# Kernel optimization log

Hardware: AMD Instinct MI355X
Metric: run time of the kernel (lower is better)

Reference implementation:

```python
import jax, jax.numpy as jnp
import numpy as np

M, N, D, L = 32, 2048, 128, 32768
H = N // D


def setup_inputs() -> dict:
    key = jax.random.key(0)
    k1, k2, k3, k4 = jax.random.split(key, 4)
    X = jax.random.normal(k1, (M, N), dtype=jnp.float32)
    # 0.02 init keeps un-scaled (no 1/sqrt(D)) logits inside fp32 exp range
    W_qkv = jax.random.normal(k2, (N, 3 * N), dtype=jnp.float32) * 0.02
    cache_K = jax.random.normal(k3, (H, L, D), dtype=jnp.float32) * 0.1
    cache_V = jax.random.normal(k4, (H, L, D), dtype=jnp.float32) * 0.1
    return {"X": X, "W_qkv": W_qkv, "cache_K": cache_K, "cache_V": cache_V, "P": 16384}


def reference(X, W_qkv, cache_K, cache_V, P):
    m, n = X.shape
    h, l, d = cache_K.shape
    # RMSNorm without learned gain, eps=0 (faithful to source)
    variance = jnp.mean(X * X, axis=-1, keepdims=True)
    X_norm = X * jax.lax.rsqrt(variance)
    # fused QKV projection: [M, 3N]
    qkv = X_norm @ W_qkv
    q, k, v = jnp.split(qkv, 3, axis=-1)
    q = q.reshape(m, h, d).transpose(1, 0, 2)  # [H, M, D]
    k = k.reshape(m, h, d).transpose(1, 0, 2)
    v = v.reshape(m, h, d).transpose(1, 0, 2)
    # KV-cache write at position P (functional update)
    cache_K = jax.lax.dynamic_update_slice(cache_K, k, (0, P, 0))
    cache_V = jax.lax.dynamic_update_slice(cache_V, v, (0, P, 0))
    # naive (non-max-subtracted, unscaled) softmax attention over full cache
    scores = jnp.einsum("hmd,hld->hml", q, cache_K)  # [H, M, L]
    scores_exp = jnp.exp(scores)
    weights = scores_exp / jnp.sum(scores_exp, axis=-1, keepdims=True)
    out = jnp.einsum("hml,hld->hmd", weights, cache_V)  # [H, M, D]
    return out.transpose(1, 0, 2).reshape(m, h * d)
```

## Files before the change

### kernel.cpp

```cpp
#include <hip/hip_runtime.h>

#define MM 32
#define NN 2048
#define NJ 6144
#define HH 16
#define DD 128
#define LL 32768

typedef __attribute__((ext_vector_type(8))) short bf16x8;
typedef __attribute__((ext_vector_type(4))) short bf16x4s;
typedef __attribute__((ext_vector_type(4))) float f32x4;

static __device__ __forceinline__ short f2bf(float f) {
    union { float f; unsigned u; } v; v.f = f;
    unsigned r = v.u + 0x7FFFu + ((v.u >> 16) & 1u);
    return (short)(r >> 16);
}

__global__ __launch_bounds__(256) void k_rms(const float* __restrict__ X,
                                             float* __restrict__ xT) {
    const int m = blockIdx.x, t = threadIdx.x;
    const float4* xr = (const float4*)(X + m * NN);
    float4 a = xr[t * 2], b = xr[t * 2 + 1];
    float s = a.x*a.x + a.y*a.y + a.z*a.z + a.w*a.w
            + b.x*b.x + b.y*b.y + b.z*b.z + b.w*b.w;
    for (int o = 32; o; o >>= 1) s += __shfl_down(s, o);
    __shared__ float red[4];
    if ((t & 63) == 0) red[t >> 6] = s;
    __syncthreads();
    float rs = rsqrtf((red[0] + red[1] + red[2] + red[3]) * (1.0f / NN));
    int n0 = t * 8;
    xT[(n0 + 0) * MM + m] = a.x * rs;
    xT[(n0 + 1) * MM + m] = a.y * rs;
    xT[(n0 + 2) * MM + m] = a.z * rs;
    xT[(n0 + 3) * MM + m] = a.w * rs;
    xT[(n0 + 4) * MM + m] = b.x * rs;
    xT[(n0 + 5) * MM + m] = b.y * rs;
    xT[(n0 + 6) * MM + m] = b.z * rs;
    xT[(n0 + 7) * MM + m] = b.w * rs;
}

__global__ __launch_bounds__(256) void k_qkv(const float* __restrict__ xT,
                                             const float* __restrict__ W,
                                             float* __restrict__ part) {
    const int j = blockIdx.x * 256 + threadIdx.x;
    const int nc = blockIdx.y;
    const int n0 = nc * 128;
    float acc[32];
#pragma unroll
    for (int m = 0; m < 32; m++) acc[m] = 0.f;
#pragma unroll 4
    for (int i = 0; i < 128; i++) {
        const float* xr = xT + (size_t)(n0 + i) * MM;
        float w = W[(size_t)(n0 + i) * NJ + j];
#pragma unroll
        for (int m = 0; m < 32; m++) acc[m] += xr[m] * w;
    }
    float* o = part + (size_t)nc * (MM * NJ) + j;
#pragma unroll
    for (int m = 0; m < 32; m++) o[(size_t)m * NJ] = acc[m];
}

__global__ __launch_bounds__(256) void k_qkvred(const float* __restrict__ part,
                                                float* __restrict__ qkv) {
    const int idx = blockIdx.x * 256 + threadIdx.x;
    float s = 0.f;
#pragma unroll
    for (int c = 0; c < 16; c++) s += part[(size_t)c * (MM * NJ) + idx];
    qkv[idx] = s;
}

#define SMEM_D 54272
__global__ __launch_bounds__(256, 1) void k_attn(const float* __restrict__ cK,
                                                 const float* __restrict__ cV,
                                                 const float* __restrict__ qkv,
                                                 const int* __restrict__ Pp,
                                                 float* __restrict__ Opart,
                                                 float* __restrict__ Dpart) {
    extern __shared__ char smem[];
    const int h = blockIdx.x, sp = blockIdx.y;
    const int t = threadIdx.x, lane = t & 63, wave = t >> 6;
    short* q_s  = (short*)smem;
    short* kv_s = (short*)(smem + 8704) + wave * (32 * 136);
    short* w_s  = (short*)(smem + 43520) + wave * (32 * 40);
    float* dred = (float*)(smem + 53760);
    const int P = *Pp;

    {
        int m = t >> 3, db = (t & 7) * 16;
        const float4* src = (const float4*)(qkv + (size_t)m * NJ + h * DD + db);
        short* dst = q_s + m * 136 + db;
#pragma unroll
        for (int k = 0; k < 4; k++) {
            float4 v = src[k];
            bf16x4s o; o.x = f2bf(v.x); o.y = f2bf(v.y); o.z = f2bf(v.z); o.w = f2bf(v.w);
            *(bf16x4s*)(dst + 4 * k) = o;
        }
    }
    __syncthreads();

    const int l15 = lane & 15, q4 = lane >> 4;
    const int row_st = lane >> 5, col4 = (lane & 31) * 4;

    bf16x8 qf[2][4];
#pragma unroll
    for (int mt = 0; mt < 2; mt++)
#pragma unroll
        for (int kb = 0; kb < 4; kb++)
            qf[mt][kb] = *(const bf16x8*)(q_s + (mt * 16 + l15) * 136 + kb * 32 + q4 * 8);

    f32x4 acc[2][8];
#pragma unroll
    for (int mt = 0; mt < 2; mt++)
#pragma unroll
        for (int dt = 0; dt < 8; dt++) acc[mt][dt] = (f32x4){0.f, 0.f, 0.f, 0.f};
    float dacc[2][4] = {{0.f,0.f,0.f,0.f},{0.f,0.f,0.f,0.f}};

    for (int c = 0; c < 8; c++) {
        const int lbase = sp * 1024 + c * 128 + wave * 32;
        {
            const float* kb_ = cK + ((size_t)h * LL + lbase) * DD + col4;
#pragma unroll 4
            for (int p = 0; p < 16; p++) {
                int row = p * 2 + row_st;
                float4 v = *(const float4*)(kb_ + (size_t)row * DD);
                bf16x4s o; o.x = f2bf(v.x); o.y = f2bf(v.y); o.z = f2bf(v.z); o.w = f2bf(v.w);
                *(bf16x4s*)(kv_s + row * 136 + col4) = o;
            }
        }
#pragma unroll
        for (int lt = 0; lt < 2; lt++) {
            const int lcol = lbase + lt * 16 + l15;
            const bool masked = ((unsigned)(lcol - P)) < 32u;
#pragma unroll
            for (int mt = 0; mt < 2; mt++) {
                f32x4 s = (f32x4){0.f, 0.f, 0.f, 0.f};
#pragma unroll
                for (int kb2 = 0; kb2 < 4; kb2++) {
                    bf16x8 bfr = *(const bf16x8*)(kv_s + (lt * 16 + l15) * 136 + kb2 * 32 + q4 * 8);
                    s = __builtin_amdgcn_mfma_f32_16x16x32_bf16(qf[mt][kb2], bfr, s, 0, 0, 0);
                }
#pragma unroll
                for (int r = 0; r < 4; r++) {
                    float e = __expf(s[r]);
                    if (masked) e = 0.f;
                    dacc[mt][r] += e;
                    w_s[(mt * 16 + q4 * 4 + r) * 40 + lt * 16 + l15] = f2bf(e);
                }
            }
        }
        {
            const float* vb_ = cV + ((size_t)h * LL + lbase) * DD + col4;
#pragma unroll 4
            for (int p = 0; p < 16; p++) {
                int row = p * 2 + row_st;
                float4 v = *(const float4*)(vb_ + (size_t)row * DD);
                bf16x4s o; o.x = f2bf(v.x); o.y = f2bf(v.y); o.z = f2bf(v.z); o.w = f2bf(v.w);
                *(bf16x4s*)(kv_s + row * 136 + col4) = o;
            }
        }
        {
            bf16x8 a0 = *(const bf16x8*)(w_s + l15 * 40 + q4 * 8);
            bf16x8 a1 = *(const bf16x8*)(w_s + (16 + l15) * 40 + q4 * 8);
#pragma unroll
            for (int dt = 0; dt < 8; dt++) {
                bf16x8 bv;
#pragma unroll
                for (int jj = 0; jj < 8; jj++)
                    bv[jj] = kv_s[(q4 * 8 + jj) * 136 + dt * 16 + l15];
                acc[0][dt] = __builtin_amdgcn_mfma_f32_16x16x32_bf16(a0, bv, acc[0][dt], 0, 0, 0);
                acc[1][dt] = __builtin_amdgcn_mfma_f32_16x16x32_bf16(a1, bv, acc[1][dt], 0, 0, 0);
            }
        }
    }

#pragma unroll
    for (int mt = 0; mt < 2; mt++)
#pragma unroll
        for (int r = 0; r < 4; r++) {
            float v = dacc[mt][r];
            v += __shfl_xor(v, 1); v += __shfl_xor(v, 2);
            v += __shfl_xor(v, 4); v += __shfl_xor(v, 8);
            if (l15 == 0) dred[wave * 32 + mt * 16 + q4 * 4 + r] = v;
        }

    __syncthreads();
    float* buf = (float*)smem;
    if (wave < 2) {
        float* ob = buf + wave * 4096;
#pragma unroll
        for (int mt = 0; mt < 2; mt++)
#pragma unroll
            for (int dt = 0; dt < 8; dt++)
#pragma unroll
                for (int r = 0; r < 4; r++)
                    ob[(mt * 16 + q4 * 4 + r) * 128 + dt * 16 + l15] = acc[mt][dt][r];
    }
    __syncthreads();
    if (wave >= 2) {
        float* ob = buf + (wave - 2) * 4096;
#pragma unroll
        for (int mt = 0; mt < 2; mt++)
#pragma unroll
            for (int dt = 0; dt < 8; dt++)
#pragma unroll
                for (int r = 0; r < 4; r++)
                    ob[(mt * 16 + q4 * 4 + r) * 128 + dt * 16 + l15] += acc[mt][dt][r];
    }
    __syncthreads();
    float* Ob = Opart + ((size_t)h * 32 + sp) * 4096;
    for (int e = t; e < 4096; e += 256) Ob[e] = buf[e] + buf[4096 + e];
    if (t < 32) {
        float d = dred[t] + dred[32 + t] + dred[64 + t] + dred[96 + t];
        Dpart[((size_t)h * 32 + sp) * 32 + t] = d;
    }
}

__global__ __launch_bounds__(128) void k_final(const float* __restrict__ qkv,
                                               const float* __restrict__ Opart,
                                               const float* __restrict__ Dpart,
                                               float* __restrict__ out) {
    const int m = blockIdx.x, h = blockIdx.y, t = threadIdx.x;
    __shared__ float wnew[32];
    if (t < 32) {
        const float* qr = qkv + (size_t)m * NJ + h * DD;
        const float* kr = qkv + (size_t)t * NJ + 2048 + h * DD;
        float s = 0.f;
#pragma unroll 8
        for (int d = 0; d < 128; d++) s += qr[d] * kr[d];
        wnew[t] = __expf(s);
    }
    __syncthreads();
    const int d = t;
    float num = 0.f, den = 0.f;
#pragma unroll 4
    for (int m2 = 0; m2 < 32; m2++) {
        num += wnew[m2] * qkv[(size_t)m2 * NJ + 4096 + h * DD + d];
        den += wnew[m2];
    }
#pragma unroll 4
    for (int s2 = 0; s2 < 32; s2++) {
        num += Opart[(((size_t)h * 32 + s2) * 32 + m) * 128 + d];
        den += Dpart[((size_t)h * 32 + s2) * 32 + m];
    }
    out[(size_t)m * NN + h * DD + d] = num / den;
}

extern "C" void kernel_launch(void* const* d_in, const int* in_sizes, int n_in,
                              void* d_out, int out_size, void* d_ws, size_t ws_size,
                              hipStream_t stream) {
    const float* X  = (const float*)d_in[0];
    const float* W  = (const float*)d_in[1];
    const float* cK = (const float*)d_in[2];
    const float* cV = (const float*)d_in[3];
    const int*   Pp = (const int*)d_in[4];
    float* ws = (float*)d_ws;

    float* xT    = ws;
    float* qpart = ws + 65536;
    float* qkv   = ws + 3211264;
    float* Opart = ws + 3407872;
    float* Dpart = ws + 5505024;

    k_rms<<<32, 256, 0, stream>>>(X, xT);
    k_qkv<<<dim3(24, 16), 256, 0, stream>>>(xT, W, qpart);
    k_qkvred<<<768, 256, 0, stream>>>(qpart, qkv);
    k_attn<<<dim3(16, 32), 256, SMEM_D, stream>>>(cK, cV, qkv, Pp, Opart, Dpart);
    k_final<<<dim3(32, 16), 128, 0, stream>>>(qkv, Opart, Dpart, (float*)d_out);
}
```

Measured before the change: 585.9 us.

## Load K fragments directly into registers and prefetch next K chunk

K tiles are now loaded from global memory straight into MFMA fragment layout in registers, skipping the LDS staging round trip. The next chunk's K is prefetched while the current V tile is converted and the PV MFMAs run, and V loads are issued early into registers. Launch bounds are raised to allow two blocks per CU. This adds register pressure, which may cause spills under the tighter launch bound, and the K loads are now less coalesced (32-byte pieces per lane).

```diff
diff --git a/kernel.cpp b/kernel.cpp
--- a/kernel.cpp
+++ b/kernel.cpp
@@ -71,7 +71,7 @@
 }
 
 #define SMEM_D 54272
-__global__ __launch_bounds__(256, 1) void k_attn(const float* __restrict__ cK,
+__global__ __launch_bounds__(256, 2) void k_attn(const float* __restrict__ cK,
                                                  const float* __restrict__ cV,
                                                  const float* __restrict__ qkv,
                                                  const int* __restrict__ Pp,
@@ -81,10 +81,26 @@
     const int h = blockIdx.x, sp = blockIdx.y;
     const int t = threadIdx.x, lane = t & 63, wave = t >> 6;
     short* q_s  = (short*)smem;
-    short* kv_s = (short*)(smem + 8704) + wave * (32 * 136);
+    short* v_s  = (short*)(smem + 8704) + wave * (32 * 136);
     short* w_s  = (short*)(smem + 43520) + wave * (32 * 40);
     float* dred = (float*)(smem + 53760);
     const int P = *Pp;
+
+    const int l15 = lane & 15, q4 = lane >> 4;
+    const int row_st = lane >> 5, col4 = (lane & 31) * 4;
+
+    const float* kbase = cK + ((size_t)h * LL + sp * 1024 + wave * 32) * DD;
+    const float* vbase = cV + ((size_t)h * LL + sp * 1024 + wave * 32) * DD;
+
+    float4 kraw[2][4][2];
+#pragma unroll
+    for (int lt = 0; lt < 2; lt++)
+#pragma unroll
+        for (int kb = 0; kb < 4; kb++) {
+            const float* p0 = kbase + (size_t)(lt * 16 + l15) * DD + kb * 32 + q4 * 8;
+            kraw[lt][kb][0] = *(const float4*)p0;
+            kraw[lt][kb][1] = *(const float4*)(p0 + 4);
+        }
 
     {
         int m = t >> 3, db = (t & 7) * 16;
@@ -99,9 +115,6 @@
     }
     __syncthreads();
 
-    const int l15 = lane & 15, q4 = lane >> 4;
-    const int row_st = lane >> 5, col4 = (lane & 31) * 4;
-
     bf16x8 qf[2][4];
 #pragma unroll
     for (int mt = 0; mt < 2; mt++)
@@ -118,16 +131,27 @@
 
     for (int c = 0; c < 8; c++) {
         const int lbase = sp * 1024 + c * 128 + wave * 32;
+
+        float4 vraw[16];
         {
-            const float* kb_ = cK + ((size_t)h * LL + lbase) * DD + col4;
-#pragma unroll 4
-            for (int p = 0; p < 16; p++) {
-                int row = p * 2 + row_st;
-                float4 v = *(const float4*)(kb_ + (size_t)row * DD);
-                bf16x4s o; o.x = f2bf(v.x); o.y = f2bf(v.y); o.z = f2bf(v.z); o.w = f2bf(v.w);
-                *(bf16x4s*)(kv_s + row * 136 + col4) = o;
+            const float* vb_ = vbase + (size_t)c * (128 * DD) + col4;
+#pragma unroll
+            for (int p = 0; p < 16; p++)
+                vraw[p] = *(const float4*)(vb_ + (size_t)(p * 2 + row_st) * DD);
+        }
+
+        bf16x8 kf[2][4];
+#pragma unroll
+        for (int lt = 0; lt < 2; lt++)
+#pragma unroll
+            for (int kb = 0; kb < 4; kb++) {
+                float4 a = kraw[lt][kb][0], b = kraw[lt][kb][1];
+                bf16x8 o;
+                o[0] = f2bf(a.x); o[1] = f2bf(a.y); o[2] = f2bf(a.z); o[3] = f2bf(a.w);
+                o[4] = f2bf(b.x); o[5] = f2bf(b.y); o[6] = f2bf(b.z); o[7] = f2bf(b.w);
+                kf[lt][kb] = o;
             }
-        }
+
 #pragma unroll
         for (int lt = 0; lt < 2; lt++) {
             const int lcol = lbase + lt * 16 + l15;
@@ -136,10 +160,8 @@
             for (int mt = 0; mt < 2; mt++) {
                 f32x4 s = (f32x4){0.f, 0.f, 0.f, 0.f};
 #pragma unroll
-                for (int kb2 = 0; kb2 < 4; kb2++) {
-                    bf16x8 bfr = *(const bf16x8*)(kv_s + (lt * 16 + l15) * 136 + kb2 * 32 + q4 * 8);
-                    s = __builtin_amdgcn_mfma_f32_16x16x32_bf16(qf[mt][kb2], bfr, s, 0, 0, 0);
-                }
+                for (int kb = 0; kb < 4; kb++)
+                    s = __builtin_amdgcn_mfma_f32_16x16x32_bf16(qf[mt][kb], kf[lt][kb], s, 0, 0, 0);
 #pragma unroll
                 for (int r = 0; r < 4; r++) {
                     float e = __expf(s[r]);
@@ -149,16 +171,26 @@
                 }
             }
         }
-        {
-            const float* vb_ = cV + ((size_t)h * LL + lbase) * DD + col4;
-#pragma unroll 4
-            for (int p = 0; p < 16; p++) {
-                int row = p * 2 + row_st;
-                float4 v = *(const float4*)(vb_ + (size_t)row * DD);
-                bf16x4s o; o.x = f2bf(v.x); o.y = f2bf(v.y); o.z = f2bf(v.z); o.w = f2bf(v.w);
-                *(bf16x4s*)(kv_s + row * 136 + col4) = o;
-            }
-        }
+
+#pragma unroll
+        for (int p = 0; p < 16; p++) {
+            float4 v = vraw[p];
+            bf16x4s o; o.x = f2bf(v.x); o.y = f2bf(v.y); o.z = f2bf(v.z); o.w = f2bf(v.w);
+            *(bf16x4s*)(v_s + (p * 2 + row_st) * 136 + col4) = o;
+        }
+
+        if (c < 7) {
+            const float* kc = kbase + (size_t)(c + 1) * (128 * DD);
+#pragma unroll
+            for (int lt = 0; lt < 2; lt++)
+#pragma unroll
+                for (int kb = 0; kb < 4; kb++) {
+                    const float* p0 = kc + (size_t)(lt * 16 + l15) * DD + kb * 32 + q4 * 8;
+                    kraw[lt][kb][0] = *(const float4*)p0;
+                    kraw[lt][kb][1] = *(const float4*)(p0 + 4);
+                }
+        }
+
         {
             bf16x8 a0 = *(const bf16x8*)(w_s + l15 * 40 + q4 * 8);
             bf16x8 a1 = *(const bf16x8*)(w_s + (16 + l15) * 40 + q4 * 8);
@@ -167,7 +199,7 @@
                 bf16x8 bv;
 #pragma unroll
                 for (int jj = 0; jj < 8; jj++)
-                    bv[jj] = kv_s[(q4 * 8 + jj) * 136 + dt * 16 + l15];
+                    bv[jj] = v_s[(q4 * 8 + jj) * 136 + dt * 16 + l15];
                 acc[0][dt] = __builtin_amdgcn_mfma_f32_16x16x32_bf16(a0, bv, acc[0][dt], 0, 0, 0);
                 acc[1][dt] = __builtin_amdgcn_mfma_f32_16x16x32_bf16(a1, bv, acc[1][dt], 0, 0, 0);
             }
```

New measurement: 582.8 us. About the same (-0.5%).
